# Kernel tuning notes

Hardware: AMD Instinct MI355X
Metric: run time of the kernel (lower is better)

The kernel has to match this reference:

```python
import jax, jax.numpy as jnp
import numpy as np

NBITS = 3      # weight LSQ bits
PBITS = 8      # partial-sum LSQ bits
EPS = 1e-5


def round_ste(x):
    # straight-through round: identity gradient
    return x + jax.lax.stop_gradient(jnp.round(x) - x)


def lsq(x, alpha, nbits):
    # learned-step-size quantize/dequantize (symmetric signed)
    qn = -(2 ** (nbits - 1))
    qp = 2 ** (nbits - 1) - 1
    return round_ste(jnp.clip(x / alpha, qn, qp)) * alpha


def split_views(x):
    # x: [B,C,H,W] -> 9 shifted views of the 1-padded input, stacked [9,B,C,H,W]
    B, C, H, W = x.shape
    xp = jnp.pad(x, ((0, 0), (0, 0), (1, 1), (1, 1)))
    views = [xp[:, :, di:di + H, dj:dj + W] for dj in range(3) for di in range(3)]
    return jnp.stack(views, 0)


def split_conv3x3(x, w, wa, pa):
    # 3x3 conv emulated as 9 shifted 1x1 LSQ convs with quantized partial-sum accumulate
    # w: [9,O,C] per-tap 1x1 weights, wa: [9] weight step sizes, pa: [9] psum step sizes
    xs = split_views(x)                                      # [9,B,C,H,W]
    wq = jax.vmap(lambda wk, ak: lsq(wk, ak, NBITS))(w, wa)  # [9,O,C]
    ps = jnp.einsum('kbchw,koc->kbohw', xs, wq)              # 9 partial sums
    psq = lsq(ps, pa[:, None, None, None, None], PBITS)      # PartialSumLSQ each tap
    return psq.sum(0)                                        # accumulate -> [B,O,H,W]


def batchnorm(x, g, b):
    m = x.mean((0, 2, 3), keepdims=True)
    v = x.var((0, 2, 3), keepdims=True)
    return (x - m) / jnp.sqrt(v + EPS) * g[None, :, None, None] + b[None, :, None, None]


def setup_inputs() -> dict:
    key = jax.random.key(0)
    ks = jax.random.split(key, 8)
    B, C, O, H, W = 16, 128, 128, 56, 56
    x = jax.random.normal(ks[0], (B, C, H, W), jnp.float32)
    w1 = jax.random.normal(ks[1], (9, O, C), jnp.float32) * 0.05
    w2 = jax.random.normal(ks[2], (9, O, O), jnp.float32) * 0.05
    qp_w = 2 ** (NBITS - 1) - 1
    wa1 = 2.0 * jnp.mean(jnp.abs(w1), axis=(1, 2)) / np.sqrt(qp_w)
    wa2 = 2.0 * jnp.mean(jnp.abs(w2), axis=(1, 2)) / np.sqrt(qp_w)
    pa1 = jnp.full((9,), 0.05, jnp.float32)
    pa2 = jnp.full((9,), 0.05, jnp.float32)
    g1 = jnp.ones((O,), jnp.float32); b1 = jnp.zeros((O,), jnp.float32)
    g2 = jnp.ones((O,), jnp.float32); b2 = jnp.zeros((O,), jnp.float32)
    return {'x': x, 'w1': w1, 'wa1': wa1, 'pa1': pa1, 'g1': g1, 'b1': b1,
            'w2': w2, 'wa2': wa2, 'pa2': pa2, 'g2': g2, 'b2': b2}


def reference(x, w1, wa1, pa1, g1, b1, w2, wa2, pa2, g2, b2):
    identity = x
    out = split_conv3x3(x, w1, wa1, pa1)
    out = jax.nn.relu(batchnorm(out, g1, b1))
    out = split_conv3x3(out, w2, wa2, pa2)
    out = batchnorm(out, g2, b2)
    return jax.nn.relu(out + identity)
```

## Files before the change

kernel.cpp:

```cpp
#include <hip/hip_runtime.h>
#include <math.h>

typedef _Float16 f16;
typedef _Float16 half8 __attribute__((ext_vector_type(8)));
typedef float floatx16 __attribute__((ext_vector_type(16)));
typedef unsigned int u32;

#define HW_     3136
#define NPC     50176.0f
#define PB      3364
#define PPLANE  53824
#define ASTRIDE (2 * PPLANE * 16)

#define SW(c, px) (((px) + ((c) >> 2) + ((c) & 3) * 8) & 63)

typedef __attribute__((address_space(3))) u32 lds_u32;
typedef __attribute__((address_space(1))) u32 glb_u32;
__device__ __forceinline__ void async_copy16(const void* g, void* l) {
    __builtin_amdgcn_global_load_lds((const glb_u32*)g, (lds_u32*)l, 16, 0, 0);
}

__global__ __launch_bounds__(256) void prep_kernel(
        const float* __restrict__ w1, const float* __restrict__ wa1,
        const float* __restrict__ w2, const float* __restrict__ wa2,
        f16* __restrict__ W2a, f16* __restrict__ W2b) {
    const int idx = blockIdx.x * 256 + threadIdx.x;
    const float* w;
    const float* wa;
    f16* o;
    int m;
    if (idx < 18432) { w = w1; wa = wa1; o = W2a; m = idx; }
    else             { w = w2; wa = wa2; o = W2b; m = idx - 18432; }
    const int tap = m >> 11;
    const int r = m & 2047;
    const int k2 = r >> 7;
    const int oc = r & 127;
    const float a = wa[tap];
    const float* src = w + ((size_t)(tap * 128 + oc) * 128 + k2 * 8);
    half8 hv;
#pragma unroll
    for (int j = 0; j < 8; ++j)
        hv[j] = (f16)rintf(fminf(fmaxf(src[j] / a, -4.f), 3.f));
    *(half8*)(o + (size_t)m * 8) = hv;
}

__global__ __launch_bounds__(256) void pad_kernel(char* __restrict__ X2) {
    const int idx = blockIdx.x * 256 + threadIdx.x;
    const int k2 = idx / 3648;
    const int r = idx - k2 * 3648;
    const int b = r / 228;
    const int j = r - b * 228;
    int h, w;
    if (j < 58)        { h = 0;  w = j; }
    else if (j < 116)  { h = 57; w = j - 58; }
    else { const int k = j - 116; h = 1 + (k >> 1); w = (k & 1) * 57; }
    const size_t chunk = (size_t)k2 * PPLANE + (size_t)b * PB + h * 58 + w;
    float4 z = {0.f, 0.f, 0.f, 0.f};
    *(float4*)(X2 + chunk * 16) = z;
}

__global__ __launch_bounds__(256) void pack_kernel(
        const float* __restrict__ x, char* __restrict__ X2,
        float* __restrict__ stats) {
    const int t = threadIdx.x;
    const int blk = blockIdx.x;
    if (blk == 0 && t < 512) stats[t] = 0.f;
    const int b = blk / 49;
    const int p0 = (blk - b * 49) * 64;
    const int px = t & 63;
    const int cq = t >> 6;
    const int p = p0 + px;
    const int h = p / 56;
    const int w = p - h * 56;
    const size_t pp = (size_t)b * PB + (h + 1) * 58 + (w + 1);
    const float* xb = x + (size_t)b * 128 * HW_ + p;
#pragma unroll
    for (int s = 0; s < 4; ++s) {
        const int cg = s * 4 + cq;
        half8 hv, lv;
#pragma unroll
        for (int j = 0; j < 8; ++j) {
            const float v = xb[(size_t)(cg * 8 + j) * HW_];
            const f16 hh = (f16)v;
            hv[j] = hh;
            lv[j] = (f16)(v - (float)hh);
        }
        *(half8*)(X2 + ((size_t)cg * PPLANE + pp) * 16) = hv;
        *(half8*)(X2 + ((size_t)(cg + 16) * PPLANE + pp) * 16) = lv;
    }
}

__global__ __launch_bounds__(256, 2) void conv_kernel(
        const char* __restrict__ X2, const char* __restrict__ W2,
        const float* __restrict__ wav, const float* __restrict__ pav,
        float* __restrict__ cbuf, float* __restrict__ stats) {
    __shared__ f16 Bls[2][16384];
    __shared__ float red[512];
    const int t = threadIdx.x;
    const int lane = t & 63;
    const int wv = t >> 6;
    const int wm = wv & 1, wn = wv >> 1;
    const int tile = (blockIdx.x & 7) * 49 + (blockIdx.x >> 3);
    const int kh = lane >> 5;
    const int ln = lane & 31;

    int ppad[2];
#pragma unroll
    for (int mt = 0; mt < 2; ++mt) {
        const int gp = tile * 128 + wm * 64 + mt * 32 + ln;
        const int b = gp / HW_;
        const int p = gp - b * HW_;
        const int h = p / 56;
        const int w = p - h * 56;
        ppad[mt] = b * PB + (h + 1) * 58 + (w + 1);
    }
    int bdsoff[2];
#pragma unroll
    for (int nt = 0; nt < 2; ++nt)
        bdsoff[nt] = (kh * 128 + wn * 64 + nt * 32 + ln) * 16;
    const int sbase = wv * 8;

    floatx16 facc[2][2];
#pragma unroll
    for (int mt = 0; mt < 2; ++mt)
#pragma unroll
        for (int nt = 0; nt < 2; ++nt)
#pragma unroll
            for (int r = 0; r < 16; ++r) facc[mt][nt][r] = 0.f;

#pragma unroll
    for (int i = 0; i < 8; ++i)
        async_copy16(W2 + (((sbase + i) * 64 + lane) << 4),
                     (void*)&Bls[0][(sbase + i) * 512]);
    int aoff[2], aoffn[2];
#pragma unroll
    for (int mt = 0; mt < 2; ++mt) {
        aoff[mt] = ((ppad[mt] - 59) + kh * PPLANE) << 4;
        aoffn[mt] = aoff[mt];
    }
    half8 afr[2][8];
#pragma unroll
    for (int s0 = 0; s0 < 8; ++s0)
#pragma unroll
        for (int mt = 0; mt < 2; ++mt)
            afr[mt][s0] = *(const half8*)(X2 + aoff[mt] + s0 * ASTRIDE);
    __syncthreads();

    for (int tap = 0; tap < 9; ++tap) {
        const float pak = pav[tap];
        const float s1 = wav[tap] / pak;
        const char* bcur = (const char*)&Bls[tap & 1][0];
        if (tap < 8) {
            const char* wt = W2 + (tap + 1) * 32768;
            f16* bnxt = &Bls[(tap + 1) & 1][0];
#pragma unroll
            for (int i = 0; i < 8; ++i)
                async_copy16(wt + (((sbase + i) * 64 + lane) << 4),
                             (void*)&bnxt[(sbase + i) * 512]);
            const int dn = ((tap + 1) % 3 - 1) * 58 + ((tap + 1) / 3 - 1);
#pragma unroll
            for (int mt = 0; mt < 2; ++mt)
                aoffn[mt] = ((ppad[mt] + dn) + kh * PPLANE) << 4;
        }
        half8 bds[2][2];
#pragma unroll
        for (int nt = 0; nt < 2; ++nt)
#pragma unroll
            for (int sl = 0; sl < 2; ++sl)
                bds[nt][sl] = *(const half8*)(bcur + sl * 4096 + bdsoff[nt]);

        floatx16 acc[2][2];
#pragma unroll
        for (int mt = 0; mt < 2; ++mt)
#pragma unroll
            for (int nt = 0; nt < 2; ++nt)
#pragma unroll
                for (int r = 0; r < 16; ++r) acc[mt][nt][r] = 0.f;

#pragma unroll
        for (int s = 0; s < 16; ++s) {
#pragma unroll
            for (int nt = 0; nt < 2; ++nt)
#pragma unroll
                for (int mt = 0; mt < 2; ++mt)
                    acc[mt][nt] = __builtin_amdgcn_mfma_f32_32x32x16_f16(
                        afr[mt][s & 7], bds[nt][s & 1], acc[mt][nt], 0, 0, 0);
            if (s <= 13) {
                const int kf2 = (s + 2) & 7;
#pragma unroll
                for (int nt = 0; nt < 2; ++nt)
                    bds[nt][s & 1] =
                        *(const half8*)(bcur + kf2 * 4096 + bdsoff[nt]);
            }
            if (s < 8) {
#pragma unroll
                for (int mt = 0; mt < 2; ++mt)
                    afr[mt][s & 7] =
                        *(const half8*)(X2 + aoff[mt] + (s + 8) * ASTRIDE);
            } else if (tap < 8) {
#pragma unroll
                for (int mt = 0; mt < 2; ++mt)
                    afr[mt][s & 7] =
                        *(const half8*)(X2 + aoffn[mt] + (s - 8) * ASTRIDE);
            }
        }

#pragma unroll
        for (int mt = 0; mt < 2; ++mt)
#pragma unroll
            for (int nt = 0; nt < 2; ++nt)
#pragma unroll
                for (int r = 0; r < 16; ++r) {
                    const float q =
                        rintf(fminf(fmaxf(acc[mt][nt][r] * s1, -128.f), 127.f));
                    facc[mt][nt][r] = fmaf(q, pak, facc[mt][nt][r]);
                }
        aoff[0] = aoffn[0];
        aoff[1] = aoffn[1];
        __syncthreads();
    }

    const int gpb = tile * 128 + wm * 64;
    const int ocb = wn * 64 + ln;
#pragma unroll
    for (int mt = 0; mt < 2; ++mt)
#pragma unroll
        for (int r = 0; r < 16; ++r) {
            const int row = (r & 3) + 8 * (r >> 2) + 4 * kh;
            const int gp = gpb + mt * 32 + row;
            float* rp = cbuf + (size_t)gp * 128 + ocb;
            rp[0]  = facc[mt][0][r];
            rp[32] = facc[mt][1][r];
        }

    float sv[2], qv[2];
#pragma unroll
    for (int nt = 0; nt < 2; ++nt) {
        float s = 0.f, q = 0.f;
#pragma unroll
        for (int mt = 0; mt < 2; ++mt)
#pragma unroll
            for (int r = 0; r < 16; ++r) {
                const float v = facc[mt][nt][r];
                s += v;
                q = fmaf(v, v, q);
            }
        s += __shfl_xor(s, 32, 64);
        q += __shfl_xor(q, 32, 64);
        sv[nt] = s; qv[nt] = q;
    }
    if (lane < 32) {
#pragma unroll
        for (int nt = 0; nt < 2; ++nt) {
            const int oc = wn * 64 + nt * 32 + lane;
            red[oc * 2 + wm] = sv[nt];
            red[256 + oc * 2 + wm] = qv[nt];
        }
    }
    __syncthreads();
    if (t < 128) {
        atomicAdd(&stats[t],       red[2 * t] + red[2 * t + 1]);
        atomicAdd(&stats[128 + t], red[256 + 2 * t] + red[256 + 2 * t + 1]);
    }
}

__global__ __launch_bounds__(256) void bn_split_kernel(
        const float* __restrict__ cbuf, const float* __restrict__ stats,
        const float* __restrict__ g, const float* __restrict__ bb,
        char* __restrict__ X2) {
    __shared__ float xs[8192];
    __shared__ float scs[128], shs[128];
    const int t = threadIdx.x;
    if (t < 128) {
        const float m = stats[t] * (1.f / NPC);
        const float var = stats[128 + t] * (1.f / NPC) - m * m;
        const float inv = 1.f / sqrtf(var + 1e-5f);
        const float sc = g[t] * inv;
        scs[t] = sc;
        shs[t] = bb[t] - m * sc;
    }
    __syncthreads();
    const int blk = blockIdx.x;
#pragma unroll
    for (int i = 0; i < 8; ++i) {
        const int idx = i * 256 + t;
        const int px = idx >> 5;
        const int q = idx & 31;
        const float4 v = *(const float4*)&cbuf[(size_t)(blk * 64 + px) * 128 + q * 4];
        const float vv[4] = {v.x, v.y, v.z, v.w};
#pragma unroll
        for (int j = 0; j < 4; ++j) {
            const int c = q * 4 + j;
            xs[c * 64 + SW(c, px)] = fmaxf(fmaf(vv[j], scs[c], shs[c]), 0.f);
        }
    }
    __syncthreads();
    const int b = blk / 49;
    const int p0 = (blk - b * 49) * 64;
    const int px = t & 63;
    const int cq = t >> 6;
    const int p = p0 + px;
    const int h = p / 56;
    const int w = p - h * 56;
    const size_t pp = (size_t)b * PB + (h + 1) * 58 + (w + 1);
#pragma unroll
    for (int s = 0; s < 4; ++s) {
        const int cg = s * 4 + cq;
        half8 hv, lv;
#pragma unroll
        for (int j = 0; j < 8; ++j) {
            const int c = cg * 8 + j;
            const float v = xs[c * 64 + SW(c, px)];
            const f16 hh = (f16)v;
            hv[j] = hh;
            lv[j] = (f16)(v - (float)hh);
        }
        *(half8*)(X2 + ((size_t)cg * PPLANE + pp) * 16) = hv;
        *(half8*)(X2 + ((size_t)(cg + 16) * PPLANE + pp) * 16) = lv;
    }
}

__global__ __launch_bounds__(256) void final_kernel(
        const float* __restrict__ cbuf, const float* __restrict__ stats,
        const float* __restrict__ g, const float* __restrict__ bb,
        const float* __restrict__ resid, float* __restrict__ out) {
    __shared__ float xs[8192];
    __shared__ float scs[128], shs[128];
    const int t = threadIdx.x;
    if (t < 128) {
        const float m = stats[t] * (1.f / NPC);
        const float var = stats[128 + t] * (1.f / NPC) - m * m;
        const float inv = 1.f / sqrtf(var + 1e-5f);
        const float sc = g[t] * inv;
        scs[t] = sc;
        shs[t] = bb[t] - m * sc;
    }
    __syncthreads();
    const int blk = blockIdx.x;
#pragma unroll
    for (int i = 0; i < 8; ++i) {
        const int idx = i * 256 + t;
        const int px = idx >> 5;
        const int q = idx & 31;
        const float4 v = *(const float4*)&cbuf[(size_t)(blk * 64 + px) * 128 + q * 4];
        const float vv[4] = {v.x, v.y, v.z, v.w};
#pragma unroll
        for (int j = 0; j < 4; ++j) {
            const int c = q * 4 + j;
            xs[c * 64 + SW(c, px)] = fmaf(vv[j], scs[c], shs[c]);
        }
    }
    __syncthreads();
    const int b = blk / 49;
    const int p0 = (blk - b * 49) * 64;
    const int lane = t & 63, wq = t >> 6;
#pragma unroll
    for (int i = 0; i < 32; ++i) {
        const int c = i * 4 + wq;
        const float v = xs[c * 64 + SW(c, lane)];
        const size_t gi = (size_t)(b * 128 + c) * HW_ + p0 + lane;
        out[gi] = fmaxf(v + resid[gi], 0.f);
    }
}

extern "C" void kernel_launch(void* const* d_in, const int* in_sizes, int n_in,
                              void* d_out, int out_size, void* d_ws, size_t ws_size,
                              hipStream_t stream) {
    const float* x   = (const float*)d_in[0];
    const float* w1  = (const float*)d_in[1];
    const float* wa1 = (const float*)d_in[2];
    const float* pa1 = (const float*)d_in[3];
    const float* g1  = (const float*)d_in[4];
    const float* b1  = (const float*)d_in[5];
    const float* w2  = (const float*)d_in[6];
    const float* wa2 = (const float*)d_in[7];
    const float* pa2 = (const float*)d_in[8];
    const float* g2  = (const float*)d_in[9];
    const float* b2  = (const float*)d_in[10];
    float* out = (float*)d_out;

    char* ws = (char*)d_ws;
    char*  X2    = ws;
    float* cbuf  = (float*)(ws + 27557888);
    f16*   W2a   = (f16*)(ws + 53248000);
    f16*   W2b   = (f16*)(ws + 53542912);
    float* stats = (float*)(ws + 53837824);
    float* stats1 = stats;
    float* stats2 = stats + 256;

    hipLaunchKernelGGL(prep_kernel, dim3(144), dim3(256), 0, stream,
                       w1, wa1, w2, wa2, W2a, W2b);
    hipLaunchKernelGGL(pad_kernel, dim3(456), dim3(256), 0, stream, X2);
    hipLaunchKernelGGL(pack_kernel, dim3(784), dim3(256), 0, stream,
                       x, X2, stats);
    hipLaunchKernelGGL(conv_kernel, dim3(392), dim3(256), 0, stream,
                       X2, (const char*)W2a, wa1, pa1, cbuf, stats1);
    hipLaunchKernelGGL(bn_split_kernel, dim3(784), dim3(256), 0, stream,
                       cbuf, stats1, g1, b1, X2);
    hipLaunchKernelGGL(conv_kernel, dim3(392), dim3(256), 0, stream,
                       X2, (const char*)W2b, wa2, pa2, cbuf, stats2);
    hipLaunchKernelGGL(final_kernel, dim3(784), dim3(256), 0, stream,
                       cbuf, stats2, g2, b2, x, out);
}
```

Measured before the change: 212.6 us.

## Halve conv M-tile, load weights straight to registers, fuse setup kernels

The conv kernel's pixel tile drops from 128 to 64 per block, which doubles the grid to 784 blocks. The LDS double-buffered weight staging and its per-tap barriers are removed, and each wave now loads its B fragments from global memory into registers, prefetching the next tap's weights during the second half of each tap. The prep, pad and pack kernels are merged into one launch. This cuts sync and LDS traffic and improves occupancy and load balance. In exchange, global weight reads per block rise and each fetched weight is reused across fewer pixels.

Result: slower. 221.0 us (+3.9%).

```diff
diff --git a/kernel.cpp b/kernel.cpp
--- a/kernel.cpp
+++ b/kernel.cpp
@@ -4,7 +4,6 @@
 typedef _Float16 f16;
 typedef _Float16 half8 __attribute__((ext_vector_type(8)));
 typedef float floatx16 __attribute__((ext_vector_type(16)));
-typedef unsigned int u32;
 
 #define HW_     3136
 #define NPC     50176.0f
@@ -14,79 +13,71 @@
 
 #define SW(c, px) (((px) + ((c) >> 2) + ((c) & 3) * 8) & 63)
 
-typedef __attribute__((address_space(3))) u32 lds_u32;
-typedef __attribute__((address_space(1))) u32 glb_u32;
-__device__ __forceinline__ void async_copy16(const void* g, void* l) {
-    __builtin_amdgcn_global_load_lds((const glb_u32*)g, (lds_u32*)l, 16, 0, 0);
-}
-
-__global__ __launch_bounds__(256) void prep_kernel(
+__global__ __launch_bounds__(256) void setup_kernel(
+        const float* __restrict__ x,
         const float* __restrict__ w1, const float* __restrict__ wa1,
         const float* __restrict__ w2, const float* __restrict__ wa2,
-        f16* __restrict__ W2a, f16* __restrict__ W2b) {
-    const int idx = blockIdx.x * 256 + threadIdx.x;
-    const float* w;
-    const float* wa;
-    f16* o;
-    int m;
-    if (idx < 18432) { w = w1; wa = wa1; o = W2a; m = idx; }
-    else             { w = w2; wa = wa2; o = W2b; m = idx - 18432; }
-    const int tap = m >> 11;
-    const int r = m & 2047;
-    const int k2 = r >> 7;
-    const int oc = r & 127;
-    const float a = wa[tap];
-    const float* src = w + ((size_t)(tap * 128 + oc) * 128 + k2 * 8);
-    half8 hv;
-#pragma unroll
-    for (int j = 0; j < 8; ++j)
-        hv[j] = (f16)rintf(fminf(fmaxf(src[j] / a, -4.f), 3.f));
-    *(half8*)(o + (size_t)m * 8) = hv;
-}
-
-__global__ __launch_bounds__(256) void pad_kernel(char* __restrict__ X2) {
-    const int idx = blockIdx.x * 256 + threadIdx.x;
-    const int k2 = idx / 3648;
-    const int r = idx - k2 * 3648;
-    const int b = r / 228;
-    const int j = r - b * 228;
-    int h, w;
-    if (j < 58)        { h = 0;  w = j; }
-    else if (j < 116)  { h = 57; w = j - 58; }
-    else { const int k = j - 116; h = 1 + (k >> 1); w = (k & 1) * 57; }
-    const size_t chunk = (size_t)k2 * PPLANE + (size_t)b * PB + h * 58 + w;
-    float4 z = {0.f, 0.f, 0.f, 0.f};
-    *(float4*)(X2 + chunk * 16) = z;
-}
-
-__global__ __launch_bounds__(256) void pack_kernel(
-        const float* __restrict__ x, char* __restrict__ X2,
+        char* __restrict__ X2, f16* __restrict__ W2a, f16* __restrict__ W2b,
         float* __restrict__ stats) {
     const int t = threadIdx.x;
     const int blk = blockIdx.x;
-    if (blk == 0 && t < 512) stats[t] = 0.f;
-    const int b = blk / 49;
-    const int p0 = (blk - b * 49) * 64;
-    const int px = t & 63;
-    const int cq = t >> 6;
-    const int p = p0 + px;
-    const int h = p / 56;
-    const int w = p - h * 56;
-    const size_t pp = (size_t)b * PB + (h + 1) * 58 + (w + 1);
-    const float* xb = x + (size_t)b * 128 * HW_ + p;
-#pragma unroll
-    for (int s = 0; s < 4; ++s) {
-        const int cg = s * 4 + cq;
-        half8 hv, lv;
-#pragma unroll
-        for (int j = 0; j < 8; ++j) {
-            const float v = xb[(size_t)(cg * 8 + j) * HW_];
-            const f16 hh = (f16)v;
-            hv[j] = hh;
-            lv[j] = (f16)(v - (float)hh);
-        }
-        *(half8*)(X2 + ((size_t)cg * PPLANE + pp) * 16) = hv;
-        *(half8*)(X2 + ((size_t)(cg + 16) * PPLANE + pp) * 16) = lv;
+    if (blk < 784) {
+        if (blk == 0 && t < 512) stats[t] = 0.f;
+        const int b = blk / 49;
+        const int p0 = (blk - b * 49) * 64;
+        const int px = t & 63;
+        const int cq = t >> 6;
+        const int p = p0 + px;
+        const int h = p / 56;
+        const int w = p - h * 56;
+        const size_t pp = (size_t)b * PB + (h + 1) * 58 + (w + 1);
+        const float* xb = x + (size_t)b * 128 * HW_ + p;
+#pragma unroll
+        for (int s = 0; s < 4; ++s) {
+            const int cg = s * 4 + cq;
+            half8 hv, lv;
+#pragma unroll
+            for (int j = 0; j < 8; ++j) {
+                const float v = xb[(size_t)(cg * 8 + j) * HW_];
+                const f16 hh = (f16)v;
+                hv[j] = hh;
+                lv[j] = (f16)(v - (float)hh);
+            }
+            *(half8*)(X2 + ((size_t)cg * PPLANE + pp) * 16) = hv;
+            *(half8*)(X2 + ((size_t)(cg + 16) * PPLANE + pp) * 16) = lv;
+        }
+    } else if (blk < 1240) {
+        const int idx = (blk - 784) * 256 + t;
+        const int k2 = idx / 3648;
+        const int r = idx - k2 * 3648;
+        const int b = r / 228;
+        const int j = r - b * 228;
+        int h, w;
+        if (j < 58)        { h = 0;  w = j; }
+        else if (j < 116)  { h = 57; w = j - 58; }
+        else { const int k = j - 116; h = 1 + (k >> 1); w = (k & 1) * 57; }
+        const size_t chunk = (size_t)k2 * PPLANE + (size_t)b * PB + h * 58 + w;
+        float4 z = {0.f, 0.f, 0.f, 0.f};
+        *(float4*)(X2 + chunk * 16) = z;
+    } else {
+        const int idx = (blk - 1240) * 256 + t;
+        const float* w;
+        const float* wa;
+        f16* o;
+        int m;
+        if (idx < 18432) { w = w1; wa = wa1; o = W2a; m = idx; }
+        else             { w = w2; wa = wa2; o = W2b; m = idx - 18432; }
+        const int tap = m >> 11;
+        const int r = m & 2047;
+        const int k2 = r >> 7;
+        const int oc = r & 127;
+        const float a = wa[tap];
+        const float* src = w + ((size_t)(tap * 128 + oc) * 128 + k2 * 8);
+        half8 hv;
+#pragma unroll
+        for (int j = 0; j < 8; ++j)
+            hv[j] = (f16)rintf(fminf(fmaxf(src[j] / a, -4.f), 3.f));
+        *(half8*)(o + (size_t)m * 8) = hv;
     }
 }
 
@@ -94,157 +85,114 @@
         const char* __restrict__ X2, const char* __restrict__ W2,
         const float* __restrict__ wav, const float* __restrict__ pav,
         float* __restrict__ cbuf, float* __restrict__ stats) {
-    __shared__ f16 Bls[2][16384];
     __shared__ float red[512];
     const int t = threadIdx.x;
     const int lane = t & 63;
     const int wv = t >> 6;
     const int wm = wv & 1, wn = wv >> 1;
-    const int tile = (blockIdx.x & 7) * 49 + (blockIdx.x >> 3);
+    const int tile = (blockIdx.x & 7) * 98 + (blockIdx.x >> 3);
     const int kh = lane >> 5;
     const int ln = lane & 31;
 
-    int ppad[2];
-#pragma unroll
-    for (int mt = 0; mt < 2; ++mt) {
-        const int gp = tile * 128 + wm * 64 + mt * 32 + ln;
+    int abase;
+    {
+        const int gp = tile * 64 + wm * 32 + ln;
         const int b = gp / HW_;
         const int p = gp - b * HW_;
         const int h = p / 56;
         const int w = p - h * 56;
-        ppad[mt] = b * PB + (h + 1) * 58 + (w + 1);
-    }
-    int bdsoff[2];
+        abase = ((b * PB + (h + 1) * 58 + (w + 1)) + kh * PPLANE) << 4;
+    }
+    int bofs[2];
 #pragma unroll
     for (int nt = 0; nt < 2; ++nt)
-        bdsoff[nt] = (kh * 128 + wn * 64 + nt * 32 + ln) * 16;
-    const int sbase = wv * 8;
-
-    floatx16 facc[2][2];
-#pragma unroll
-    for (int mt = 0; mt < 2; ++mt)
+        bofs[nt] = (kh * 128 + wn * 64 + nt * 32 + ln) << 4;
+
+    floatx16 facc[2];
+#pragma unroll
+    for (int nt = 0; nt < 2; ++nt)
+#pragma unroll
+        for (int r = 0; r < 16; ++r) facc[nt][r] = 0.f;
+
+    int aoff = abase + (-59 << 4);
+    int aoffn = aoff;
+    half8 afr[8];
+#pragma unroll
+    for (int s0 = 0; s0 < 8; ++s0)
+        afr[s0] = *(const half8*)(X2 + aoff + s0 * ASTRIDE);
+    half8 bfr[2][8];
+#pragma unroll
+    for (int kf = 0; kf < 8; ++kf)
 #pragma unroll
         for (int nt = 0; nt < 2; ++nt)
-#pragma unroll
-            for (int r = 0; r < 16; ++r) facc[mt][nt][r] = 0.f;
-
-#pragma unroll
-    for (int i = 0; i < 8; ++i)
-        async_copy16(W2 + (((sbase + i) * 64 + lane) << 4),
-                     (void*)&Bls[0][(sbase + i) * 512]);
-    int aoff[2], aoffn[2];
-#pragma unroll
-    for (int mt = 0; mt < 2; ++mt) {
-        aoff[mt] = ((ppad[mt] - 59) + kh * PPLANE) << 4;
-        aoffn[mt] = aoff[mt];
-    }
-    half8 afr[2][8];
-#pragma unroll
-    for (int s0 = 0; s0 < 8; ++s0)
-#pragma unroll
-        for (int mt = 0; mt < 2; ++mt)
-            afr[mt][s0] = *(const half8*)(X2 + aoff[mt] + s0 * ASTRIDE);
-    __syncthreads();
-
+            bfr[nt][kf] = *(const half8*)(W2 + bofs[nt] + kf * 4096);
+
+#pragma unroll
     for (int tap = 0; tap < 9; ++tap) {
         const float pak = pav[tap];
         const float s1 = wav[tap] / pak;
-        const char* bcur = (const char*)&Bls[tap & 1][0];
         if (tap < 8) {
-            const char* wt = W2 + (tap + 1) * 32768;
-            f16* bnxt = &Bls[(tap + 1) & 1][0];
-#pragma unroll
-            for (int i = 0; i < 8; ++i)
-                async_copy16(wt + (((sbase + i) * 64 + lane) << 4),
-                             (void*)&bnxt[(sbase + i) * 512]);
             const int dn = ((tap + 1) % 3 - 1) * 58 + ((tap + 1) / 3 - 1);
-#pragma unroll
-            for (int mt = 0; mt < 2; ++mt)
-                aoffn[mt] = ((ppad[mt] + dn) + kh * PPLANE) << 4;
-        }
-        half8 bds[2][2];
+            aoffn = abase + (dn << 4);
+        }
+        const char* wtn = W2 + (tap + 1) * 32768;
+
+        floatx16 acc[2];
 #pragma unroll
         for (int nt = 0; nt < 2; ++nt)
 #pragma unroll
-            for (int sl = 0; sl < 2; ++sl)
-                bds[nt][sl] = *(const half8*)(bcur + sl * 4096 + bdsoff[nt]);
-
-        floatx16 acc[2][2];
-#pragma unroll
-        for (int mt = 0; mt < 2; ++mt)
+            for (int r = 0; r < 16; ++r) acc[nt][r] = 0.f;
+
+#pragma unroll
+        for (int s = 0; s < 16; ++s) {
 #pragma unroll
             for (int nt = 0; nt < 2; ++nt)
-#pragma unroll
-                for (int r = 0; r < 16; ++r) acc[mt][nt][r] = 0.f;
-
-#pragma unroll
-        for (int s = 0; s < 16; ++s) {
-#pragma unroll
-            for (int nt = 0; nt < 2; ++nt)
-#pragma unroll
-                for (int mt = 0; mt < 2; ++mt)
-                    acc[mt][nt] = __builtin_amdgcn_mfma_f32_32x32x16_f16(
-                        afr[mt][s & 7], bds[nt][s & 1], acc[mt][nt], 0, 0, 0);
-            if (s <= 13) {
-                const int kf2 = (s + 2) & 7;
+                acc[nt] = __builtin_amdgcn_mfma_f32_32x32x16_f16(
+                    afr[s & 7], bfr[nt][s & 7], acc[nt], 0, 0, 0);
+            if (s < 8) {
+                afr[s & 7] = *(const half8*)(X2 + aoff + (s + 8) * ASTRIDE);
+            } else if (tap < 8) {
+                afr[s & 7] = *(const half8*)(X2 + aoffn + (s - 8) * ASTRIDE);
+            }
+            if (tap < 8 && s >= 8) {
+                const int kf = s - 8;
 #pragma unroll
                 for (int nt = 0; nt < 2; ++nt)
-                    bds[nt][s & 1] =
-                        *(const half8*)(bcur + kf2 * 4096 + bdsoff[nt]);
+                    bfr[nt][kf] = *(const half8*)(wtn + bofs[nt] + kf * 4096);
             }
-            if (s < 8) {
-#pragma unroll
-                for (int mt = 0; mt < 2; ++mt)
-                    afr[mt][s & 7] =
-                        *(const half8*)(X2 + aoff[mt] + (s + 8) * ASTRIDE);
-            } else if (tap < 8) {
-#pragma unroll
-                for (int mt = 0; mt < 2; ++mt)
-                    afr[mt][s & 7] =
-                        *(const half8*)(X2 + aoffn[mt] + (s - 8) * ASTRIDE);
+        }
+
+#pragma unroll
+        for (int nt = 0; nt < 2; ++nt)
+#pragma unroll
+            for (int r = 0; r < 16; ++r) {
+                const float q =
+                    rintf(fminf(fmaxf(acc[nt][r] * s1, -128.f), 127.f));
+                facc[nt][r] = fmaf(q, pak, facc[nt][r]);
             }
-        }
-
-#pragma unroll
-        for (int mt = 0; mt < 2; ++mt)
-#pragma unroll
-            for (int nt = 0; nt < 2; ++nt)
-#pragma unroll
-                for (int r = 0; r < 16; ++r) {
-                    const float q =
-                        rintf(fminf(fmaxf(acc[mt][nt][r] * s1, -128.f), 127.f));
-                    facc[mt][nt][r] = fmaf(q, pak, facc[mt][nt][r]);
-                }
-        aoff[0] = aoffn[0];
-        aoff[1] = aoffn[1];
-        __syncthreads();
-    }
-
-    const int gpb = tile * 128 + wm * 64;
+        aoff = aoffn;
+    }
+
+    const int gpb = tile * 64 + wm * 32;
     const int ocb = wn * 64 + ln;
 #pragma unroll
-    for (int mt = 0; mt < 2; ++mt)
-#pragma unroll
-        for (int r = 0; r < 16; ++r) {
-            const int row = (r & 3) + 8 * (r >> 2) + 4 * kh;
-            const int gp = gpb + mt * 32 + row;
-            float* rp = cbuf + (size_t)gp * 128 + ocb;
-            rp[0]  = facc[mt][0][r];
-            rp[32] = facc[mt][1][r];
-        }
+    for (int r = 0; r < 16; ++r) {
+        const int row = (r & 3) + 8 * (r >> 2) + 4 * kh;
+        float* rp = cbuf + (size_t)(gpb + row) * 128 + ocb;
+        rp[0]  = facc[0][r];
+        rp[32] = facc[1][r];
+    }
 
     float sv[2], qv[2];
 #pragma unroll
     for (int nt = 0; nt < 2; ++nt) {
         float s = 0.f, q = 0.f;
 #pragma unroll
-        for (int mt = 0; mt < 2; ++mt)
-#pragma unroll
-            for (int r = 0; r < 16; ++r) {
-                const float v = facc[mt][nt][r];
-                s += v;
-                q = fmaf(v, v, q);
-            }
+        for (int r = 0; r < 16; ++r) {
+            const float v = facc[nt][r];
+            s += v;
+            q = fmaf(v, v, q);
+        }
         s += __shfl_xor(s, 32, 64);
         q += __shfl_xor(q, 32, 64);
         sv[nt] = s; qv[nt] = q;
@@ -388,16 +336,13 @@
     float* stats1 = stats;
     float* stats2 = stats + 256;
 
-    hipLaunchKernelGGL(prep_kernel, dim3(144), dim3(256), 0, stream,
-                       w1, wa1, w2, wa2, W2a, W2b);
-    hipLaunchKernelGGL(pad_kernel, dim3(456), dim3(256), 0, stream, X2);
-    hipLaunchKernelGGL(pack_kernel, dim3(784), dim3(256), 0, stream,
-                       x, X2, stats);
-    hipLaunchKernelGGL(conv_kernel, dim3(392), dim3(256), 0, stream,
+    hipLaunchKernelGGL(setup_kernel, dim3(1384), dim3(256), 0, stream,
+                       x, w1, wa1, w2, wa2, X2, W2a, W2b, stats);
+    hipLaunchKernelGGL(conv_kernel, dim3(784), dim3(256), 0, stream,
                        X2, (const char*)W2a, wa1, pa1, cbuf, stats1);
     hipLaunchKernelGGL(bn_split_kernel, dim3(784), dim3(256), 0, stream,
                        cbuf, stats1, g1, b1, X2);
-    hipLaunchKernelGGL(conv_kernel, dim3(392), dim3(256), 0, stream,
+    hipLaunchKernelGGL(conv_kernel, dim3(784), dim3(256), 0, stream,
                        X2, (const char*)W2b, wa2, pa2, cbuf, stats2);
     hipLaunchKernelGGL(final_kernel, dim3(784), dim3(256), 0, stream,
                        cbuf, stats2, g2, b2, x, out);
```
